# Optimization experiments

Hardware: AMD Instinct MI355X
Metric: run time of the kernel (lower is better)

## Reference

```python
import jax, jax.numpy as jnp
import numpy as np

V, L, H, D, T, B = 32000, 8, 16, 1024, 1024, 2
HD = D // H
SCALE = 1.0 / float(np.sqrt(HD))


def setup_inputs() -> dict:
    key = jax.random.key(0)
    ks = jax.random.split(key, 8)
    s = 0.02
    def n(k, shape):
        return jax.random.normal(k, shape, jnp.float32) * s
    return {
        "input_ids": jax.random.randint(ks[0], (B, T), 0, V),
        "tok_emb": n(ks[1], (V, D)),            # tied with lm_head
        "pos_emb": n(ks[2], (T, D)),
        "ln1_w": jnp.ones((L, D)), "ln1_b": jnp.zeros((L, D)),
        "qkv_w": n(ks[3], (L, D, 3 * D)),       # no bias in qkv_proj
        "out_w": n(ks[4], (L, D, D)), "out_b": jnp.zeros((L, D)),
        "ln2_w": jnp.ones((L, D)), "ln2_b": jnp.zeros((L, D)),
        "fc1_w": n(ks[5], (L, D, 4 * D)), "fc1_b": jnp.zeros((L, 4 * D)),
        "fc2_w": n(ks[6], (L, 4 * D, D)), "fc2_b": jnp.zeros((L, D)),
        "lnf_w": jnp.ones((D,)), "lnf_b": jnp.zeros((D,)),
    }


def _ln(x, w, b):
    m = x.mean(-1, keepdims=True)
    v = x.var(-1, keepdims=True)
    return (x - m) * jax.lax.rsqrt(v + 1e-5) * w + b


def _gpt(input_ids, tok_emb, pos_emb, ln1_w, ln1_b, qkv_w, out_w, out_b,
         ln2_w, ln2_b, fc1_w, fc1_b, fc2_w, fc2_b, lnf_w, lnf_b):
    Bq, Tq = input_ids.shape
    x = tok_emb[input_ids] + pos_emb[:Tq][None]          # [B,T,D]
    causal = jnp.tril(jnp.ones((Tq, Tq), bool))          # [T,T]

    def layer(x, p):
        l1w, l1b, qw, ow, ob, l2w, l2b, f1w, f1b, f2w, f2b = p
        h = _ln(x, l1w, l1b)
        qkv = h @ qw                                     # [B,T,3D]
        q, k, v = jnp.split(qkv, 3, axis=-1)
        q = q.reshape(Bq, Tq, H, HD)
        k = k.reshape(Bq, Tq, H, HD)
        v = v.reshape(Bq, Tq, H, HD)
        att = jnp.einsum('bqhd,bkhd->bhqk', q, k) * SCALE
        att = jnp.where(causal, att, -jnp.inf)
        att = jax.nn.softmax(att, axis=-1)
        o = jnp.einsum('bhqk,bkhd->bqhd', att, v).reshape(Bq, Tq, D)
        x = x + o @ ow + ob
        h2 = _ln(x, l2w, l2b)
        x = x + jax.nn.gelu(h2 @ f1w + f1b, approximate=False) @ f2w + f2b
        return x, None

    x, _ = jax.lax.scan(layer, x, (ln1_w, ln1_b, qkv_w, out_w, out_b,
                                   ln2_w, ln2_b, fc1_w, fc1_b, fc2_w, fc2_b))
    x = _ln(x, lnf_w, lnf_b)
    return x @ tok_emb.T                                 # tied lm_head


def reference(input_ids, tok_emb, pos_emb, ln1_w, ln1_b, qkv_w, out_w, out_b,
              ln2_w, ln2_b, fc1_w, fc1_b, fc2_w, fc2_b, lnf_w, lnf_b):
    return _gpt(input_ids, tok_emb, pos_emb, ln1_w, ln1_b, qkv_w, out_w, out_b,
                ln2_w, ln2_b, fc1_w, fc1_b, fc2_w, fc2_b, lnf_w, lnf_b)
```

## Files before the change

### kernel.cpp

```cpp
#include <hip/hip_runtime.h>
#include <hip/hip_bf16.h>
#include <math.h>


#define DEV_INLINE __device__ __forceinline__

typedef float  f32x4  __attribute__((ext_vector_type(4)));
typedef __bf16 bf16x8 __attribute__((ext_vector_type(8)));
typedef short  s16x4  __attribute__((ext_vector_type(4)));
typedef short  s16x8  __attribute__((ext_vector_type(8)));
typedef unsigned int u32x4 __attribute__((ext_vector_type(4)));

#define BBATCH 2
#define TSEQ   1024
#define DMODEL 1024
#define NHEAD  16
#define HDIM   64
#define NLAYER 8
#define NVOCAB 32000
#define MTOK   (BBATCH*TSEQ)

DEV_INLINE short f2bf(float f) {
    __bf16 h = (__bf16)f;
    union { __bf16 h; short s; } u; u.h = h; return u.s;
}

typedef const __attribute__((address_space(1))) unsigned int* gas_t;
typedef __attribute__((address_space(3))) unsigned int* las_t;
DEV_INLINE void llds16(const void* g, void* l) {
    __builtin_amdgcn_global_load_lds((gas_t)g, (las_t)l, 16, 0, 0);
}

#define BAR()  asm volatile("s_barrier" ::: "memory")
#define VMW4() asm volatile("s_waitcnt vmcnt(4)" ::: "memory")
#define VMW2() asm volatile("s_waitcnt vmcnt(2)" ::: "memory")
#define VMW0() asm volatile("s_waitcnt vmcnt(0)" ::: "memory")

DEV_INLINE float block_sum(float v) {
    __shared__ float sb[4];
    #pragma unroll
    for (int o = 32; o > 0; o >>= 1) v += __shfl_down(v, o, 64);
    if ((threadIdx.x & 63) == 0) sb[threadIdx.x >> 6] = v;
    __syncthreads();
    float r = sb[0] + sb[1] + sb[2] + sb[3];
    __syncthreads();
    return r;
}

__global__ __launch_bounds__(256) void flash_k(
    const short* __restrict__ qkv, const short* __restrict__ Vt,
    short* __restrict__ O)
{
    const int qb = blockIdx.x;
    const int z  = blockIdx.y;
    const int zb = z >> 4, zh = z & 15;

    __shared__ short Qs[128 * 64];
    __shared__ short KP[128 * 136];
    __shared__ short Vs[64 * 128];

    const int tid  = threadIdx.x;
    const int w    = tid >> 6, lane = tid & 63;
    const int lr   = lane & 15, kg = lane >> 4;

    const long long qbase = (long long)zb * TSEQ * 3072;
    const short* Qg = qkv + qbase + zh * HDIM;
    const short* Kg = qkv + qbase + DMODEL + zh * HDIM;
    const short* Vg = Vt + (long long)z * (HDIM * TSEQ);

    const int sr   = tid >> 3, pc = tid & 7;
    const int lc   = pc ^ (sr & 7);
    const int sr16 = tid >> 4, pc16 = tid & 15;

    {
        const short* qp = Qg + (long long)(qb * 128 + sr) * 3072 + lc * 8;
        const short* kp = Kg + (long long)(0 + sr) * 3072 + lc * 8;
        #pragma unroll
        for (int it = 0; it < 4; ++it) {
            llds16(qp + (long long)it * 32 * 3072, Qs + tid * 8 + it * 2048);
            llds16(kp + (long long)it * 32 * 3072, KP + tid * 8 + it * 2048);
        }
        #pragma unroll
        for (int it = 0; it < 4; ++it) {
            const int r = it * 16 + sr16;
            const int lc2 = pc16 ^ (r & 7);
            llds16(Vg + (long long)r * TSEQ + 0 + lc2 * 8, Vs + tid * 8 + it * 2048);
        }
    }
    __syncthreads();
    bf16x8 afq[2][2];
    #pragma unroll
    for (int s = 0; s < 2; ++s)
        #pragma unroll
        for (int i = 0; i < 2; ++i) {
            const int r = w * 32 + i * 16 + lr;
            afq[s][i] = *(const bf16x8*)&Qs[r * 64 + (((s * 4 + kg) ^ (r & 7)) << 3)];
        }

    f32x4 aco[2][4] = {};
    float m_[2][4], l_[2][4];
    #pragma unroll
    for (int i = 0; i < 2; ++i)
        #pragma unroll
        for (int p = 0; p < 4; ++p) { m_[i][p] = -1e30f; l_[i][p] = 0.f; }

    const int nt = qb + 1;
    for (int t = 0; t < nt; ++t) {
        u32x4 kpre[4], vpre[4];
        const bool nx = (t + 1 < nt);
        if (nx) {
            const int kn = (t + 1) * 128;
            #pragma unroll
            for (int it = 0; it < 4; ++it)
                kpre[it] = *(const u32x4*)(Kg + (long long)(kn + sr + it * 32) * 3072 + lc * 8);
            #pragma unroll
            for (int it = 0; it < 4; ++it) {
                const int r = it * 16 + sr16;
                const int lc2 = pc16 ^ (r & 7);
                vpre[it] = *(const u32x4*)(Vg + (long long)r * TSEQ + kn + lc2 * 8);
            }
            __builtin_amdgcn_sched_barrier(0);
        }

        f32x4 acs[2][8] = {};
        #pragma unroll
        for (int s = 0; s < 2; ++s)
            #pragma unroll
            for (int j = 0; j < 8; ++j) {
                const int rk = j * 16 + lr;
                bf16x8 bk = *(const bf16x8*)&KP[rk * 64 + (((s * 4 + kg) ^ (rk & 7)) << 3)];
                #pragma unroll
                for (int i = 0; i < 2; ++i)
                    acs[i][j] = __builtin_amdgcn_mfma_f32_16x16x32_bf16(
                        afq[s][i], bk, acs[i][j], 0, 0, 0);
            }

        #pragma unroll
        for (int i = 0; i < 2; ++i)
            #pragma unroll
            for (int j = 0; j < 8; ++j)
                #pragma unroll
                for (int p = 0; p < 4; ++p) {
                    float v = acs[i][j][p] * 0.125f;
                    if (t == qb && (j * 16 + lr) > (w * 32 + i * 16 + kg * 4 + p))
                        v = -1e30f;
                    acs[i][j][p] = v;
                }

        float sc[2][4];
        #pragma unroll
        for (int i = 0; i < 2; ++i)
            #pragma unroll
            for (int p = 0; p < 4; ++p) {
                float r = acs[i][0][p];
                #pragma unroll
                for (int j = 1; j < 8; ++j) r = fmaxf(r, acs[i][j][p]);
                r = fmaxf(r, __shfl_xor(r, 1, 64));
                r = fmaxf(r, __shfl_xor(r, 2, 64));
                r = fmaxf(r, __shfl_xor(r, 4, 64));
                r = fmaxf(r, __shfl_xor(r, 8, 64));
                const float mn = fmaxf(m_[i][p], r);
                sc[i][p] = __expf(m_[i][p] - mn);
                m_[i][p] = mn;
            }
        #pragma unroll
        for (int i = 0; i < 2; ++i)
            #pragma unroll
            for (int j = 0; j < 8; ++j)
                #pragma unroll
                for (int p = 0; p < 4; ++p)
                    acs[i][j][p] = __expf(acs[i][j][p] - m_[i][p]);
        #pragma unroll
        for (int i = 0; i < 2; ++i)
            #pragma unroll
            for (int p = 0; p < 4; ++p) {
                float s = 0.f;
                #pragma unroll
                for (int j = 0; j < 8; ++j) s += acs[i][j][p];
                s += __shfl_xor(s, 1, 64);
                s += __shfl_xor(s, 2, 64);
                s += __shfl_xor(s, 4, 64);
                s += __shfl_xor(s, 8, 64);
                l_[i][p] = l_[i][p] * sc[i][p] + s;
            }
        #pragma unroll
        for (int i = 0; i < 2; ++i)
            #pragma unroll
            for (int j2 = 0; j2 < 4; ++j2)
                #pragma unroll
                for (int p = 0; p < 4; ++p)
                    aco[i][j2][p] *= sc[i][p];

        __syncthreads();

        #pragma unroll
        for (int i = 0; i < 2; ++i)
            #pragma unroll
            for (int j = 0; j < 8; ++j)
                #pragma unroll
                for (int p = 0; p < 4; ++p)
                    KP[(w * 32 + i * 16 + kg * 4 + p) * 136 + j * 16 + lr] =
                        f2bf(acs[i][j][p]);
        __syncthreads();

        #pragma unroll
        for (int ks = 0; ks < 4; ++ks) {
            bf16x8 pa[2], pb[4];
            #pragma unroll
            for (int i = 0; i < 2; ++i)
                pa[i] = *(const bf16x8*)&KP[(w * 32 + i * 16 + lr) * 136 + ks * 32 + kg * 8];
            #pragma unroll
            for (int j2 = 0; j2 < 4; ++j2) {
                const int d = j2 * 16 + lr;
                pb[j2] = *(const bf16x8*)&Vs[d * 128 + (((ks * 4 + kg) ^ (d & 7)) << 3)];
            }
            #pragma unroll
            for (int i = 0; i < 2; ++i)
                #pragma unroll
                for (int j2 = 0; j2 < 4; ++j2)
                    aco[i][j2] = __builtin_amdgcn_mfma_f32_16x16x32_bf16(
                        pa[i], pb[j2], aco[i][j2], 0, 0, 0);
        }
        __syncthreads();

        if (nx) {
            #pragma unroll
            for (int it = 0; it < 4; ++it)
                *(u32x4*)(KP + tid * 8 + it * 2048) = kpre[it];
            #pragma unroll
            for (int it = 0; it < 4; ++it)
                *(u32x4*)(Vs + tid * 8 + it * 2048) = vpre[it];
            __syncthreads();
        }
    }

    #pragma unroll
    for (int i = 0; i < 2; ++i)
        #pragma unroll
        for (int j2 = 0; j2 < 4; ++j2)
            #pragma unroll
            for (int p = 0; p < 4; ++p) {
                const int row = zb * TSEQ + qb * 128 + w * 32 + i * 16 + kg * 4 + p;
                const int col = zh * HDIM + j2 * 16 + lr;
                O[(long long)row * DMODEL + col] = f2bf(aco[i][j2][p] / l_[i][p]);
            }
}

__global__ __launch_bounds__(512, 2) void gemm256_k(
    const short* __restrict__ A, const short* __restrict__ B,
    float* __restrict__ C, int K, int lda, int ldb, int ldc, int gx)
{
    extern __shared__ short smem[];

    const int nwg = gridDim.x;
    int wg = blockIdx.x;
    int sw = (wg & 7) * (nwg >> 3) + (wg >> 3);
    const int bx = sw >> 3, by = sw & 7;
    const int bn0 = bx * 256, bm0 = by * 256;

    const int tid  = threadIdx.x;
    const int w    = tid >> 6, lane = tid & 63;
    const int wm   = w >> 2, wn = w & 3;
    const int lr   = lane & 15, kg = lane >> 4;

    const int r0  = tid >> 3;
    const int pc  = tid & 7;
    const int lc0 = pc ^ (r0 & 7);
    const int r1  = r0 + 64;
    const int lc1 = pc ^ (r1 & 7);

    f32x4 acc[2][2][4][2] = {};
    const int nk = K >> 6;

    auto stage = [&](int buf, int isA, int h, int kk) {
        const short* gp = isA ? A : B;
        const int    ld = isA ? lda : ldb;
        const long long rb = (long long)((isA ? bm0 : bn0) + h * 128);
        short* lp = smem + buf * 32768 + (isA ? 0 : 16384) + h * 8192;
        llds16(gp + (rb + r0) * ld + kk + lc0 * 8, lp + w * 512);
        llds16(gp + (rb + r1) * ld + kk + lc1 * 8, lp + 4096 + w * 512);
    };

#define PHASE(BUF, QM, QN, ISA, H, DOWAIT)                                      \
    do {                                                                        \
        const short* Ah = smem + (BUF) * 32768 + (QM) * 8192;                   \
        const short* Bh = smem + (BUF) * 32768 + 16384 + (QN) * 8192;           \
        bf16x8 af[2][4], bfr[2][2];                                             \
        _Pragma("unroll")                                                       \
        for (int s2 = 0; s2 < 2; ++s2) {                                        \
            _Pragma("unroll")                                                   \
            for (int i = 0; i < 4; ++i) {                                       \
                const int ra = wm * 64 + i * 16 + lr;                           \
                af[s2][i] = *(const bf16x8*)                                    \
                    &Ah[ra * 64 + (((s2 * 4 + kg) ^ (ra & 7)) << 3)];           \
            }                                                                   \
            _Pragma("unroll")                                                   \
            for (int j = 0; j < 2; ++j) {                                       \
                const int rb2 = wn * 32 + j * 16 + lr;                          \
                bfr[s2][j] = *(const bf16x8*)                                   \
                    &Bh[rb2 * 64 + (((s2 * 4 + kg) ^ (rb2 & 7)) << 3)];         \
            }                                                                   \
        }                                                                       \
        if (pf) stage(nb, ISA, H, kk);                                          \
        BAR();                                                                  \
        __builtin_amdgcn_s_setprio(1);                                          \
        _Pragma("unroll")                                                       \
        for (int s2 = 0; s2 < 2; ++s2)                                          \
            _Pragma("unroll")                                                   \
            for (int i = 0; i < 4; ++i)                                         \
                _Pragma("unroll")                                               \
                for (int j = 0; j < 2; ++j)                                     \
                    acc[QM][QN][i][j] = __builtin_amdgcn_mfma_f32_16x16x32_bf16(\
                        bfr[s2][j], af[s2][i], acc[QM][QN][i][j], 0, 0, 0);     \
        __builtin_amdgcn_s_setprio(0);                                          \
        DOWAIT;                                                                 \
        BAR();                                                                  \
    } while (0)

    stage(0, 1, 0, 0);
    stage(0, 0, 0, 0);
    stage(0, 1, 1, 0);
    stage(0, 0, 1, 0);
    if (nk > 1) { VMW4(); } else { VMW0(); }
    BAR();

    for (int t = 0; t < nk - 1; ++t) {
        const int  buf = t & 1, nb = buf ^ 1;
        const int  kk  = (t + 1) << 6;
        const bool pf  = true;
        PHASE(buf, 0, 0, 1, 0, VMW4());
        PHASE(buf, 1, 0, 0, 0, VMW4());
        PHASE(buf, 1, 1, 1, 1, (void)0);
        PHASE(buf, 0, 1, 0, 1, VMW4());
    }
    {
        const int  buf = (nk - 1) & 1, nb = buf ^ 1; (void)nb;
        const int  kk  = 0;
        const bool pf  = false;
        PHASE(buf, 0, 0, 1, 0, VMW2());
        PHASE(buf, 1, 0, 0, 0, VMW0());
        PHASE(buf, 1, 1, 1, 1, (void)0);
        PHASE(buf, 0, 1, 0, 1, (void)0);
    }
#undef PHASE

    #pragma unroll
    for (int qm = 0; qm < 2; ++qm)
        #pragma unroll
        for (int qn = 0; qn < 2; ++qn)
            #pragma unroll
            for (int i = 0; i < 4; ++i)
                #pragma unroll
                for (int j = 0; j < 2; ++j) {
                    const int gr  = bm0 + qm * 128 + wm * 64 + i * 16 + lr;
                    const int gc0 = bn0 + qn * 128 + wn * 32 + j * 16 + kg * 4;
                    *(float4*)&C[(long long)gr * ldc + gc0] =
                        *(const float4*)&acc[qm][qn][i][j];
                }
}

template<int BN, int EPI>
__global__ __launch_bounds__(256) void gemm_k(
    const short* __restrict__ Ag, const short* __restrict__ Bg,
    void* __restrict__ Cg, const float* __restrict__ bias,
    short* __restrict__ aux,
    int M, int N, int K, int lda, int ldb, int ldc,
    long long sAz, long long sBz, long long sCz,
    float scale, int swz)
{
    int bx = blockIdx.x, by = blockIdx.y;
    if (swz) {
        const int gx = gridDim.x;
        const int nwg = gx * gridDim.y;
        if ((nwg & 7) == 0) {
            int wg = by * gx + bx;
            int wg2 = (wg & 7) * (nwg >> 3) + (wg >> 3);
            bx = wg2 % gx; by = wg2 / gx;
        }
    }
    const int bn0 = bx * BN, bm0 = by * 128;
    const int zz = blockIdx.z;

    const short* A = Ag + zz * sAz;
    const short* B = Bg + zz * sBz;

    __shared__ short Als[2][128 * 64];
    __shared__ short Bls[2][BN * 64];

    const int tid  = threadIdx.x;
    const int lane = tid & 63;
    const int wave = tid >> 6;
    constexpr int WMS = (BN == 128) ? 64 : 32;
    constexpr int MI  = (BN == 128) ? 4 : 2;
    constexpr int NJ  = 4;
    constexpr bool SW = (EPI == 0 || EPI == 3);
    const int wm = (BN == 128) ? (wave >> 1) : wave;
    const int wn = (BN == 128) ? (wave & 1) : 0;
    const int lr = lane & 15, kg = lane >> 4;
    const int xv = (lr & 7) << 4;

    const int sr = tid >> 3;
    const int sc = (tid & 7) ^ (sr & 7);
    const short* aP = A + (long long)(bm0 + sr) * lda + sc * 8;
    const short* bP = B + (long long)(bn0 + sr) * ldb + sc * 8;

    f32x4 acc[MI][NJ] = {};
    const int nk = K >> 6;

    auto stage = [&](int buf, int kt) {
        const int k0 = kt << 6;
        short* aL = &Als[buf][wave * 512];
        short* bL = &Bls[buf][wave * 512];
        #pragma unroll
        for (int it = 0; it < 4; ++it)
            llds16(aP + (long long)it * 32 * lda + k0, aL + it * 2048);
        #pragma unroll
        for (int it = 0; it < BN / 32; ++it)
            llds16(bP + (long long)it * 32 * ldb + k0, bL + it * 2048);
    };

    stage(0, 0);
    __syncthreads();

    for (int kt = 0; kt < nk; ++kt) {
        const int cb = kt & 1;
        if (kt + 1 < nk) stage(cb ^ 1, kt + 1);

        #pragma unroll
        for (int s = 0; s < 2; ++s) {
            const int ofs = (((s << 6) | (kg << 4)) ^ xv) >> 1;
            bf16x8 af[MI], bf[NJ];
            #pragma unroll
            for (int i = 0; i < MI; ++i)
                af[i] = *(const bf16x8*)&Als[cb][(wm * WMS + i * 16 + lr) * 64 + ofs];
            #pragma unroll
            for (int j = 0; j < NJ; ++j)
                bf[j] = *(const bf16x8*)&Bls[cb][(wn * 64 + j * 16 + lr) * 64 + ofs];
            #pragma unroll
            for (int i = 0; i < MI; ++i)
                #pragma unroll
                for (int j = 0; j < NJ; ++j) {
                    if (SW)
                        acc[i][j] = __builtin_amdgcn_mfma_f32_16x16x32_bf16(
                            bf[j], af[i], acc[i][j], 0, 0, 0);
                    else
                        acc[i][j] = __builtin_amdgcn_mfma_f32_16x16x32_bf16(
                            af[i], bf[j], acc[i][j], 0, 0, 0);
                }
        }
        __syncthreads();
    }

    short* Cs = (short*)Cg + zz * sCz;
    float* Cf = (float*)Cg + zz * sCz;
    #pragma unroll
    for (int i = 0; i < MI; ++i) {
        #pragma unroll
        for (int j = 0; j < NJ; ++j) {
            if (SW) {
                const int gr  = bm0 + wm * WMS + i * 16 + lr;
                const int gc0 = bn0 + wn * 64 + j * 16 + kg * 4;
                if (EPI == 0) {
                    *(float4*)&Cf[(long long)gr * ldc + gc0] =
                        *(const float4*)&acc[i][j];
                } else {
                    float4 bb = *(const float4*)&bias[gc0];
                    s16x4 ov;
                    #pragma unroll
                    for (int p = 0; p < 4; ++p) {
                        float v = acc[i][j][p] + ((const float*)&bb)[p];
                        v = 0.5f * v * (1.0f + erff(v * 0.70710678118654752f));
                        ov[p] = f2bf(v);
                    }
                    *(s16x4*)&Cs[(long long)gr * ldc + gc0] = ov;
                }
            } else {
                const int gr = bm0 + wm * WMS + i * 16 + kg * 4;
                const int gc = bn0 + wn * 64 + j * 16 + lr;
                if (EPI == 4 && gc >= 2 * DMODEL) {
                    const int b = gr >> 10, t0 = gr & (TSEQ - 1);
                    const int h = (gc - 2 * DMODEL) >> 6, d = gc & 63;
                    s16x4 vv;
                    #pragma unroll
                    for (int p = 0; p < 4; ++p) vv[p] = f2bf(acc[i][j][p]);
                    *(s16x4*)&aux[((long long)(b * NHEAD + h) * HDIM + d) * TSEQ + t0] = vv;
                } else {
                    #pragma unroll
                    for (int p = 0; p < 4; ++p)
                        Cs[(long long)(gr + p) * ldc + gc] = f2bf(acc[i][j][p] * scale);
                }
            }
        }
    }
}

template<int NP>
__global__ __launch_bounds__(256) void fredln_k(
    const float* __restrict__ fp, long long pstride,
    const float* __restrict__ bias, float* __restrict__ x,
    const float* __restrict__ lw, const float* __restrict__ lb,
    short* __restrict__ o)
{
    const int row  = blockIdx.x * 4 + (threadIdx.x >> 6);
    const int lane = threadIdx.x & 63;
    const long long base = (long long)row * DMODEL + lane * 16;
    const int cb = lane * 16;
    float4 v[4];
    #pragma unroll
    for (int q = 0; q < 4; ++q) {
        v[q] = *(const float4*)&x[base + q * 4];
        float4 bb = *(const float4*)&bias[cb + q * 4];
        v[q].x += bb.x; v[q].y += bb.y; v[q].z += bb.z; v[q].w += bb.w;
        #pragma unroll
        for (int k = 0; k < NP; ++k) {
            float4 pp = *(const float4*)&fp[k * pstride + base + q * 4];
            v[q].x += pp.x; v[q].y += pp.y; v[q].z += pp.z; v[q].w += pp.w;
        }
        *(float4*)&x[base + q * 4] = v[q];
    }
    float s = 0.f, s2 = 0.f;
    #pragma unroll
    for (int q = 0; q < 4; ++q) {
        s  += v[q].x + v[q].y + v[q].z + v[q].w;
        s2 += v[q].x * v[q].x + v[q].y * v[q].y + v[q].z * v[q].z + v[q].w * v[q].w;
    }
    #pragma unroll
    for (int d = 1; d < 64; d <<= 1) {
        s  += __shfl_xor(s, d, 64);
        s2 += __shfl_xor(s2, d, 64);
    }
    const float mean = s * (1.0f / DMODEL);
    const float var  = s2 * (1.0f / DMODEL) - mean * mean;
    const float rs   = rsqrtf(var + 1e-5f);
    short ov[16];
    #pragma unroll
    for (int q = 0; q < 4; ++q) {
        float4 wv = *(const float4*)&lw[cb + q * 4];
        float4 bv = *(const float4*)&lb[cb + q * 4];
        ov[q * 4 + 0] = f2bf((v[q].x - mean) * rs * wv.x + bv.x);
        ov[q * 4 + 1] = f2bf((v[q].y - mean) * rs * wv.y + bv.y);
        ov[q * 4 + 2] = f2bf((v[q].z - mean) * rs * wv.z + bv.z);
        ov[q * 4 + 3] = f2bf((v[q].w - mean) * rs * wv.w + bv.w);
    }
    short* op = o + base;
    *(s16x8*)op       = *(s16x8*)&ov[0];
    *(s16x8*)(op + 8) = *(s16x8*)&ov[8];
}

__global__ __launch_bounds__(256) void embedln_k(
    const int* __restrict__ ids, const float* __restrict__ tok,
    const float* __restrict__ pos, float* __restrict__ x,
    const float* __restrict__ lw, const float* __restrict__ lb,
    short* __restrict__ o)
{
    const int row = blockIdx.x;
    const int t   = row & (TSEQ - 1);
    const int id  = ids[row];
    const int i   = threadIdx.x * 4;
    const long long base = (long long)row * DMODEL;
    float4 a = *(const float4*)&tok[(long long)id * DMODEL + i];
    float4 p = *(const float4*)&pos[(long long)t * DMODEL + i];
    float4 v;
    v.x = a.x + p.x; v.y = a.y + p.y; v.z = a.z + p.z; v.w = a.w + p.w;
    *(float4*)&x[base + i] = v;
    float s  = v.x + v.y + v.z + v.w;
    float s2 = v.x * v.x + v.y * v.y + v.z * v.z + v.w * v.w;
    s  = block_sum(s);
    s2 = block_sum(s2);
    const float mean = s * (1.0f / DMODEL);
    const float var  = s2 * (1.0f / DMODEL) - mean * mean;
    const float rs   = rsqrtf(var + 1e-5f);
    float4 wv = *(const float4*)&lw[i];
    float4 bv = *(const float4*)&lb[i];
    s16x4 ov;
    ov[0] = f2bf((v.x - mean) * rs * wv.x + bv.x);
    ov[1] = f2bf((v.y - mean) * rs * wv.y + bv.y);
    ov[2] = f2bf((v.z - mean) * rs * wv.z + bv.z);
    ov[3] = f2bf((v.w - mean) * rs * wv.w + bv.w);
    *(s16x4*)&o[base + i] = ov;
}

template<typename T>
DEV_INLINE void tcvt_body(const T* sp, short* dp, int lds_, int ldd,
                          int bx, int by, short (*ls)[68], int t)
{
    const int tr0 = by * 64, tc0 = bx * 64;
    const int rr = t >> 4, cc = (t & 15) * 4;
    #pragma unroll
    for (int q = 0; q < 4; ++q) {
        const int r = q * 16 + rr;
        if constexpr (sizeof(T) == 4) {
            float4 v = *(const float4*)&sp[(long long)(tr0 + r) * lds_ + tc0 + cc];
            ls[cc + 0][r] = f2bf(v.x); ls[cc + 1][r] = f2bf(v.y);
            ls[cc + 2][r] = f2bf(v.z); ls[cc + 3][r] = f2bf(v.w);
        } else {
            s16x4 v = *(const s16x4*)&sp[(long long)(tr0 + r) * lds_ + tc0 + cc];
            ls[cc + 0][r] = v[0]; ls[cc + 1][r] = v[1];
            ls[cc + 2][r] = v[2]; ls[cc + 3][r] = v[3];
        }
    }
    __syncthreads();
    #pragma unroll
    for (int q = 0; q < 4; ++q) {
        const int c = q * 16 + rr;
        s16x4 v;
        v[0] = ls[c][cc]; v[1] = ls[c][cc + 1]; v[2] = ls[c][cc + 2]; v[3] = ls[c][cc + 3];
        *(s16x4*)&dp[(long long)(tc0 + c) * ldd + tr0 + cc] = v;
    }
}

template<typename T>
__global__ __launch_bounds__(256) void tcvt_k(
    const T* __restrict__ src, short* __restrict__ dst,
    int lds_, int ldd, int Hdiv,
    long long sSb, long long sSh, long long sDb, long long sDh)
{
    __shared__ short ls[64][68];
    const int z = blockIdx.z, zb = z / Hdiv, zh = z - zb * Hdiv;
    tcvt_body<T>(src + zb * sSb + zh * sSh, dst + zb * sDb + zh * sDh,
                 lds_, ldd, blockIdx.x, blockIdx.y, ls, threadIdx.x);
}

__global__ __launch_bounds__(256) void wcvt_k(
    const float* __restrict__ qw, const float* __restrict__ ow,
    const float* __restrict__ f1, const float* __restrict__ f2,
    short* __restrict__ wq, short* __restrict__ wo,
    short* __restrict__ w1, short* __restrict__ w2)
{
    __shared__ short ls[64][68];
    const int id = blockIdx.x;
    const float* src; short* dst; int lds_, ldd, bx, by;
    if (id < 768)       { src = qw; dst = wq; lds_ = 3072; ldd = 1024; bx = id % 48;  by = id / 48; }
    else if (id < 1024) { int i = id - 768;  src = ow; dst = wo; lds_ = 1024; ldd = 1024; bx = i % 16; by = i / 16; }
    else if (id < 2048) { int i = id - 1024; src = f1; dst = w1; lds_ = 4096; ldd = 1024; bx = i % 64; by = i / 64; }
    else                { int i = id - 2048; src = f2; dst = w2; lds_ = 1024; ldd = 4096; bx = i % 16; by = i / 16; }
    tcvt_body<float>(src, dst, lds_, ldd, bx, by, ls, threadIdx.x);
}

__global__ __launch_bounds__(256) void cvt_k(
    const float* __restrict__ s, short* __restrict__ d, int n4)
{
    int i = blockIdx.x * 256 + threadIdx.x;
    const int stride = gridDim.x * 256;
    for (; i < n4; i += stride) {
        float4 v = *(const float4*)&s[(long long)i * 4];
        s16x4 o = { f2bf(v.x), f2bf(v.y), f2bf(v.z), f2bf(v.w) };
        *(s16x4*)&d[(long long)i * 4] = o;
    }
}

extern "C" void kernel_launch(void* const* d_in, const int* in_sizes, int n_in,
                              void* d_out, int out_size, void* d_ws, size_t ws_size,
                              hipStream_t stream)
{
    const int*   ids  = (const int*)  d_in[0];
    const float* tok  = (const float*)d_in[1];
    const float* pos  = (const float*)d_in[2];
    const float* ln1w = (const float*)d_in[3];
    const float* ln1b = (const float*)d_in[4];
    const float* qkvw = (const float*)d_in[5];
    const float* outw = (const float*)d_in[6];
    const float* outb = (const float*)d_in[7];
    const float* ln2w = (const float*)d_in[8];
    const float* ln2b = (const float*)d_in[9];
    const float* fc1w = (const float*)d_in[10];
    const float* fc1b = (const float*)d_in[11];
    const float* fc2w = (const float*)d_in[12];
    const float* fc2b = (const float*)d_in[13];
    const float* lnfw = (const float*)d_in[14];
    const float* lnfb = (const float*)d_in[15];
    float* out = (float*)d_out;

    char* ws = (char*)d_ws;
    const size_t MB = 1024 * 1024;
    float* x    = (float*)(ws);
    short* hb   = (short*)(ws + 8  * MB);
    short* qkvb = (short*)(ws + 12 * MB);
    short* g    = (short*)(ws + 24 * MB);
    short* Vt   = (short*)(ws + 40 * MB);
    float* fp   = (float*)(ws + 44 * MB);
    short* tokb = (short*)(ws + 12 * MB);

    const bool big = ws_size >= (size_t)272 * MB;
    short* wq = (short*)(ws + 80 * MB);
    short *wo, *w1, *w2;
    if (big) {
        wo = (short*)(ws + 128 * MB);
        w1 = (short*)(ws + 144 * MB);
        w2 = (short*)(ws + 208 * MB);
    } else {
        wo = (short*)(ws + 86 * MB);
        w1 = (short*)(ws + 88 * MB);
        w2 = (short*)(ws + 96 * MB);
    }

    const long long LWQ = 3072LL * 1024, LWO = 1024LL * 1024;
    const long long LW1 = 4096LL * 1024, LW2 = 1024LL * 4096;
    const long long MD  = (long long)MTOK * DMODEL;

    hipFuncSetAttribute((const void*)gemm256_k,
                        hipFuncAttributeMaxDynamicSharedMemorySize, 131072);

    dim3 blk(256);
    embedln_k<<<MTOK, blk, 0, stream>>>(ids, tok, pos, x, ln1w, ln1b, hb);

    if (big) {
        tcvt_k<float><<<dim3(48, 16, 8), blk, 0, stream>>>(qkvw, wq, 3072, 1024, 1, LWQ, 0, LWQ, 0);
        tcvt_k<float><<<dim3(16, 16, 8), blk, 0, stream>>>(outw, wo, 1024, 1024, 1, LWO, 0, LWO, 0);
        tcvt_k<float><<<dim3(64, 16, 8), blk, 0, stream>>>(fc1w, w1, 4096, 1024, 1, LW1, 0, LW1, 0);
        tcvt_k<float><<<dim3(16, 64, 8), blk, 0, stream>>>(fc2w, w2, 1024, 4096, 1, LW2, 0, LW2, 0);
    }

    for (int l = 0; l < NLAYER; ++l) {
        short* wql = wq + (big ? l * LWQ : 0);
        short* wol = wo + (big ? l * LWO : 0);
        short* w1l = w1 + (big ? l * LW1 : 0);
        short* w2l = w2 + (big ? l * LW2 : 0);
        if (!big)
            wcvt_k<<<3072, blk, 0, stream>>>(
                qkvw + l * LWQ, outw + l * LWO, fc1w + l * LW1, fc2w + l * LW2,
                wql, wol, w1l, w2l);

        gemm_k<128, 4><<<dim3(24, 16, 1), blk, 0, stream>>>(
            hb, wql, qkvb, nullptr, Vt,
            MTOK, 3 * DMODEL, DMODEL, DMODEL, DMODEL, 3 * DMODEL,
            0, 0, 0, 1.0f, 1);

        flash_k<<<dim3(8, BBATCH * NHEAD), blk, 0, stream>>>(qkvb, Vt, hb);

        gemm_k<128, 0><<<dim3(8, 16, 2), blk, 0, stream>>>(
            hb, wol, fp, nullptr, nullptr,
            MTOK, DMODEL, 512, DMODEL, DMODEL, DMODEL,
            512, 512, MD, 1.0f, 1);
        fredln_k<2><<<MTOK / 4, blk, 0, stream>>>(
            fp, MD, outb + l * DMODEL, x,
            ln2w + l * DMODEL, ln2b + l * DMODEL, hb);

        gemm_k<128, 3><<<dim3(32, 16, 1), blk, 0, stream>>>(
            hb, w1l, g, fc1b + (long long)l * 4 * DMODEL, nullptr,
            MTOK, 4 * DMODEL, DMODEL, DMODEL, DMODEL, 4 * DMODEL,
            0, 0, 0, 1.0f, 1);

        gemm_k<128, 0><<<dim3(8, 16, 4), blk, 0, stream>>>(
            g, w2l, fp, nullptr, nullptr,
            MTOK, DMODEL, 1024, 4 * DMODEL, 4 * DMODEL, DMODEL,
            1024, 1024, MD, 1.0f, 1);
        const float* nlw = (l < 7) ? ln1w + (l + 1) * DMODEL : lnfw;
        const float* nlb = (l < 7) ? ln1b + (l + 1) * DMODEL : lnfb;
        fredln_k<4><<<MTOK / 4, blk, 0, stream>>>(
            fp, MD, fc2b + l * DMODEL, x, nlw, nlb, hb);
    }

    cvt_k<<<2048, blk, 0, stream>>>(tok, tokb, NVOCAB * DMODEL / 4);

    gemm256_k<<<dim3((NVOCAB / 256) * (MTOK / 256)), dim3(512), 131072, stream>>>(
        hb, tokb, out, DMODEL, DMODEL, DMODEL, NVOCAB, NVOCAB / 256);
}
```

Baseline: 1.592 ms.

## Store split-K partials in bf16 and swap MFMA operands in lm_head GEMM

The split-K out-projection and fc2 GEMMs now write their partial sums as bf16 through a new epilogue, and the fused residual/LayerNorm kernel reads those bf16 partials. This halves the bytes written and re-read for the partials. It also rounds each partial to bf16 before accumulation, which loses precision. The lm_head GEMM's MFMA operands are swapped, so its output is now written with scalar per-row stores instead of float4 stores. That change alters the write pattern of the largest output tensor.

```diff
diff --git a/kernel.cpp b/kernel.cpp
--- a/kernel.cpp
+++ b/kernel.cpp
@@ -23,6 +23,10 @@
 DEV_INLINE short f2bf(float f) {
     __bf16 h = (__bf16)f;
     union { __bf16 h; short s; } u; u.h = h; return u.s;
+}
+DEV_INLINE float bf2f(short s) {
+    union { unsigned u; float f; } x; x.u = ((unsigned)(unsigned short)s) << 16;
+    return x.f;
 }
 
 typedef const __attribute__((address_space(1))) unsigned int* gas_t;
@@ -311,7 +315,7 @@
                 _Pragma("unroll")                                               \
                 for (int j = 0; j < 2; ++j)                                     \
                     acc[QM][QN][i][j] = __builtin_amdgcn_mfma_f32_16x16x32_bf16(\
-                        bfr[s2][j], af[s2][i], acc[QM][QN][i][j], 0, 0, 0);     \
+                        af[s2][i], bfr[s2][j], acc[QM][QN][i][j], 0, 0, 0);     \
         __builtin_amdgcn_s_setprio(0);                                          \
         DOWAIT;                                                                 \
         BAR();                                                                  \
@@ -352,10 +356,11 @@
             for (int i = 0; i < 4; ++i)
                 #pragma unroll
                 for (int j = 0; j < 2; ++j) {
-                    const int gr  = bm0 + qm * 128 + wm * 64 + i * 16 + lr;
-                    const int gc0 = bn0 + qn * 128 + wn * 32 + j * 16 + kg * 4;
-                    *(float4*)&C[(long long)gr * ldc + gc0] =
-                        *(const float4*)&acc[qm][qn][i][j];
+                    const int gr = bm0 + qm * 128 + wm * 64 + i * 16 + kg * 4;
+                    const int gc = bn0 + qn * 128 + wn * 32 + j * 16 + lr;
+                    #pragma unroll
+                    for (int p = 0; p < 4; ++p)
+                        C[(long long)(gr + p) * ldc + gc] = acc[qm][qn][i][j][p];
                 }
 }
 
@@ -393,7 +398,7 @@
     constexpr int WMS = (BN == 128) ? 64 : 32;
     constexpr int MI  = (BN == 128) ? 4 : 2;
     constexpr int NJ  = 4;
-    constexpr bool SW = (EPI == 0 || EPI == 3);
+    constexpr bool SW = (EPI == 0 || EPI == 3 || EPI == 5);
     const int wm = (BN == 128) ? (wave >> 1) : wave;
     const int wn = (BN == 128) ? (wave & 1) : 0;
     const int lr = lane & 15, kg = lane >> 4;
@@ -463,6 +468,11 @@
                 if (EPI == 0) {
                     *(float4*)&Cf[(long long)gr * ldc + gc0] =
                         *(const float4*)&acc[i][j];
+                } else if (EPI == 5) {
+                    s16x4 ov;
+                    #pragma unroll
+                    for (int p = 0; p < 4; ++p) ov[p] = f2bf(acc[i][j][p]);
+                    *(s16x4*)&Cs[(long long)gr * ldc + gc0] = ov;
                 } else {
                     float4 bb = *(const float4*)&bias[gc0];
                     s16x4 ov;
@@ -496,7 +506,7 @@
 
 template<int NP>
 __global__ __launch_bounds__(256) void fredln_k(
-    const float* __restrict__ fp, long long pstride,
+    const short* __restrict__ fp, long long pstride,
     const float* __restrict__ bias, float* __restrict__ x,
     const float* __restrict__ lw, const float* __restrict__ lb,
     short* __restrict__ o)
@@ -511,13 +521,25 @@
         v[q] = *(const float4*)&x[base + q * 4];
         float4 bb = *(const float4*)&bias[cb + q * 4];
         v[q].x += bb.x; v[q].y += bb.y; v[q].z += bb.z; v[q].w += bb.w;
-        #pragma unroll
-        for (int k = 0; k < NP; ++k) {
-            float4 pp = *(const float4*)&fp[k * pstride + base + q * 4];
-            v[q].x += pp.x; v[q].y += pp.y; v[q].z += pp.z; v[q].w += pp.w;
-        }
+    }
+    #pragma unroll
+    for (int k = 0; k < NP; ++k) {
+        const short* pp = &fp[k * pstride + base];
+        s16x8 p0 = *(const s16x8*)pp;
+        s16x8 p1 = *(const s16x8*)(pp + 8);
+        #pragma unroll
+        for (int q = 0; q < 4; ++q) {
+            const int e = q * 4;
+            float e0 = bf2f((e + 0 < 8) ? p0[e + 0] : p1[e + 0 - 8]);
+            float e1 = bf2f((e + 1 < 8) ? p0[e + 1] : p1[e + 1 - 8]);
+            float e2 = bf2f((e + 2 < 8) ? p0[e + 2] : p1[e + 2 - 8]);
+            float e3 = bf2f((e + 3 < 8) ? p0[e + 3] : p1[e + 3 - 8]);
+            v[q].x += e0; v[q].y += e1; v[q].z += e2; v[q].w += e3;
+        }
+    }
+    #pragma unroll
+    for (int q = 0; q < 4; ++q)
         *(float4*)&x[base + q * 4] = v[q];
-    }
     float s = 0.f, s2 = 0.f;
     #pragma unroll
     for (int q = 0; q < 4; ++q) {
@@ -678,7 +700,7 @@
     short* qkvb = (short*)(ws + 12 * MB);
     short* g    = (short*)(ws + 24 * MB);
     short* Vt   = (short*)(ws + 40 * MB);
-    float* fp   = (float*)(ws + 44 * MB);
+    short* fp   = (short*)(ws + 44 * MB);
     short* tokb = (short*)(ws + 12 * MB);
 
     const bool big = ws_size >= (size_t)272 * MB;
@@ -728,7 +750,7 @@
 
         flash_k<<<dim3(8, BBATCH * NHEAD), blk, 0, stream>>>(qkvb, Vt, hb);
 
-        gemm_k<128, 0><<<dim3(8, 16, 2), blk, 0, stream>>>(
+        gemm_k<128, 5><<<dim3(8, 16, 2), blk, 0, stream>>>(
             hb, wol, fp, nullptr, nullptr,
             MTOK, DMODEL, 512, DMODEL, DMODEL, DMODEL,
             512, 512, MD, 1.0f, 1);
@@ -741,7 +763,7 @@
             MTOK, 4 * DMODEL, DMODEL, DMODEL, DMODEL, 4 * DMODEL,
             0, 0, 0, 1.0f, 1);
 
-        gemm_k<128, 0><<<dim3(8, 16, 4), blk, 0, stream>>>(
+        gemm_k<128, 5><<<dim3(8, 16, 4), blk, 0, stream>>>(
             g, w2l, fp, nullptr, nullptr,
             MTOK, DMODEL, 1024, 4 * DMODEL, 4 * DMODEL, DMODEL,
             1024, 1024, MD, 1.0f, 1);
```

Result: faster. 1.551 ms (median of 2 runs) (-2.6%).
